# Kernel tuning notes

Measured on AMD Instinct MI355X. Metric: run time of the kernel, lower is better.

## Reference

```python
import jax, jax.numpy as jnp
import numpy as np

D_IN = 1024
D_OUT = 1024
H = 16


def setup_inputs() -> dict:
    key = jax.random.key(0)
    ks = jax.random.split(key, 11)
    B, Tq, Tk = 2, 2048, 2048
    s = 1.0 / np.sqrt(D_IN)
    return {
        "q": jax.random.normal(ks[0], (B, Tq, D_IN), jnp.float32),
        "k": jax.random.normal(ks[1], (B, Tk, D_IN), jnp.float32),
        "v": jax.random.normal(ks[2], (B, Tk, D_IN), jnp.float32),
        "Wq": jax.random.uniform(ks[3], (D_IN, D_OUT), jnp.float32, -s, s),
        "bq": jax.random.uniform(ks[4], (D_OUT,), jnp.float32, -s, s),
        "Wk": jax.random.uniform(ks[5], (D_IN, D_OUT), jnp.float32, -s, s),
        "bk": jax.random.uniform(ks[6], (D_OUT,), jnp.float32, -s, s),
        "Wv": jax.random.uniform(ks[7], (D_IN, D_OUT), jnp.float32, -s, s),
        "bv": jax.random.uniform(ks[8], (D_OUT,), jnp.float32, -s, s),
        "Wo": jax.random.uniform(ks[9], (D_OUT, D_OUT), jnp.float32, -s, s),
        "bo": jax.random.uniform(ks[10], (D_OUT,), jnp.float32, -s, s),
    }


def reference(q, k, v, Wq, bq, Wk, bk, Wv, bv, Wo, bo):
    B, Tq, _ = q.shape
    Tk = k.shape[1]
    hd = D_OUT // H
    # QKV projections, split heads -> [B, H, T, hd]
    qh = (q @ Wq + bq).reshape(B, Tq, H, hd).transpose(0, 2, 1, 3)
    kh = (k @ Wk + bk).reshape(B, Tk, H, hd).transpose(0, 2, 1, 3)
    vh = (v @ Wv + bv).reshape(B, Tk, H, hd).transpose(0, 2, 1, 3)
    # scaled dot-product attention (scale uses key dim = head_dim)
    scores = jnp.einsum("bhqd,bhkd->bhqk", qh, kh) / jnp.sqrt(jnp.float32(hd))
    attn = jax.nn.softmax(scores, axis=-1)
    x = jnp.einsum("bhqk,bhkd->bhqd", attn, vh)
    x = x.transpose(0, 2, 1, 3).reshape(B, Tq, D_OUT)
    return x @ Wo + bo
```

## Files before the change

### kernel.cpp

```cpp
#include <hip/hip_runtime.h>
#include <hip/hip_bf16.h>

typedef __attribute__((ext_vector_type(8))) short short8;
typedef __attribute__((ext_vector_type(4))) short short4v;
typedef __attribute__((ext_vector_type(4))) float f32x4;

__device__ __forceinline__ unsigned short f2bf(float f) {
    __hip_bfloat16 h = __float2bfloat16(f);
    unsigned short u;
    __builtin_memcpy(&u, &h, 2);
    return u;
}
__device__ __forceinline__ short4v pack4bf(float a, float b, float c, float d) {
    union { __hip_bfloat162 h[2]; short4v s; } r;
    r.h[0] = __float22bfloat162_rn(make_float2(a, b));
    r.h[1] = __float22bfloat162_rn(make_float2(c, d));
    return r.s;
}
union cat8 { short4v h[2]; short8 v8; };

#define GLD16(gp, lp) __builtin_amdgcn_global_load_lds( \
    (const __attribute__((address_space(1))) void*)(gp), \
    (__attribute__((address_space(3))) void*)(lp), 16, 0, 0)

#define PHASE(WAITN) do { \
        asm volatile("s_waitcnt vmcnt(" #WAITN ")" ::: "memory"); \
        __builtin_amdgcn_s_barrier(); \
        asm volatile("" ::: "memory"); \
        __builtin_amdgcn_sched_barrier(0); } while (0)

__global__ __launch_bounds__(256) void prep(
    const float* __restrict__ q, const float* __restrict__ k, const float* __restrict__ v,
    unsigned short* __restrict__ qb, unsigned short* __restrict__ kb, unsigned short* __restrict__ vb,
    const float* __restrict__ W0, const float* __restrict__ W1,
    const float* __restrict__ W2, const float* __restrict__ W3,
    unsigned short* __restrict__ T0, unsigned short* __restrict__ T1,
    unsigned short* __restrict__ T2, unsigned short* __restrict__ T3)
{
    __shared__ unsigned short Ts[64 * 68];
    int bx = blockIdx.x;
    if (bx < 6144) {
        const float* src; unsigned short* dst;
        switch (bx >> 11) { case 0: src = q; dst = qb; break;
                            case 1: src = k; dst = kb; break;
                            default: src = v; dst = vb; break; }
        size_t i = ((size_t)(bx & 2047) * 256 + threadIdx.x) * 8;
        float4 x0 = *(const float4*)&src[i];
        float4 x1 = *(const float4*)&src[i + 4];
        union { unsigned short s[8]; uint4 u; } p;
        p.s[0] = f2bf(x0.x); p.s[1] = f2bf(x0.y); p.s[2] = f2bf(x0.z); p.s[3] = f2bf(x0.w);
        p.s[4] = f2bf(x1.x); p.s[5] = f2bf(x1.y); p.s[6] = f2bf(x1.z); p.s[7] = f2bf(x1.w);
        *(uint4*)&dst[i] = p.u;
        return;
    }
    int w = bx - 6144;
    int z = w >> 8, rem = w & 255;
    int kx = rem >> 4, ny = rem & 15;
    const float* W;
    unsigned short* T;
    switch (z) {
        case 0: W = W0; T = T0; break;
        case 1: W = W1; T = T1; break;
        case 2: W = W2; T = T2; break;
        default: W = W3; T = T3; break;
    }
    int tid = threadIdx.x;
    int c = tid & 7, r = tid >> 3;
    int k0 = kx * 64, n0 = ny * 64;
    for (int i = 0; i < 64; i += 32) {
        const float* src = &W[(size_t)(k0 + r + i) * 1024 + n0 + c * 8];
        float4 x0 = *(const float4*)src;
        float4 x1 = *(const float4*)(src + 4);
        unsigned short* d = &Ts[(r + i) * 68 + c * 8];
        d[0] = f2bf(x0.x); d[1] = f2bf(x0.y); d[2] = f2bf(x0.z); d[3] = f2bf(x0.w);
        d[4] = f2bf(x1.x); d[5] = f2bf(x1.y); d[6] = f2bf(x1.z); d[7] = f2bf(x1.w);
    }
    __syncthreads();
    for (int i = 0; i < 64; i += 32) {
        union { unsigned short s[8]; uint4 v; } u;
        for (int j = 0; j < 8; j++) u.s[j] = Ts[(c * 8 + j) * 68 + (r + i)];
        *(uint4*)&T[(size_t)(n0 + r + i) * 1024 + k0 + c * 8] = u.v;
    }
}

__device__ __forceinline__ void gemm_core_p(
    const unsigned short* __restrict__ A, const unsigned short* __restrict__ BT,
    const float* __restrict__ bias, unsigned short* __restrict__ out16,
    int mode, float scale)
{
    const int K = 1024;
    __shared__ unsigned short As[3][128 * 32];
    __shared__ unsigned short Bs[3][128 * 32];
    int tid = threadIdx.x;
    int m0 = blockIdx.x * 128, n0 = blockIdx.y * 128;
    int lane = tid & 63, wave = tid >> 6;
    int lm = lane & 15, quad = lane >> 4;
    int wm = (wave >> 1) * 64, wn = (wave & 1) * 64;

    int lrow = lane >> 2;
    int scol = ((lane & 3) ^ ((lane >> 3) & 3)) * 8;
    const unsigned short* Ag = A + (size_t)(m0 + wave * 32 + lrow) * K + scol;
    const unsigned short* Bg = BT + (size_t)(n0 + wave * 32 + lrow) * K + scol;

    int rpos = (quad ^ ((lm >> 1) & 3)) * 8;

    f32x4 acc[4][4];
    for (int i = 0; i < 4; i++)
        for (int j = 0; j < 4; j++)
            for (int r = 0; r < 4; r++) acc[i][j][r] = 0.0f;

#define GSTAGE(BUF) do { \
        GLD16(Ag,          &As[BUF][(wave * 32) * 32]); \
        GLD16(Ag + 16 * K, &As[BUF][(wave * 32 + 16) * 32]); \
        GLD16(Bg,          &Bs[BUF][(wave * 32) * 32]); \
        GLD16(Bg + 16 * K, &Bs[BUF][(wave * 32 + 16) * 32]); \
        Ag += 32; Bg += 32; } while (0)

#define GCOMP(BUF) do { \
        short8 a[4], b[4]; \
        _Pragma("unroll") \
        for (int i = 0; i < 4; i++) \
            a[i] = *(const short8*)&As[BUF][(wm + i * 16 + lm) * 32 + rpos]; \
        _Pragma("unroll") \
        for (int j = 0; j < 4; j++) \
            b[j] = *(const short8*)&Bs[BUF][(wn + j * 16 + lm) * 32 + rpos]; \
        _Pragma("unroll") \
        for (int i = 0; i < 4; i++) \
            _Pragma("unroll") \
            for (int j = 0; j < 4; j++) \
                acc[i][j] = __builtin_amdgcn_mfma_f32_16x16x32_bf16(a[i], b[j], acc[i][j], 0, 0, 0); \
        } while (0)

    GSTAGE(0); GSTAGE(1);
    for (int u = 0; u < 10; u++) {
        PHASE(4); GSTAGE(2); GCOMP(0);
        PHASE(4); GSTAGE(0); GCOMP(1);
        PHASE(4); GSTAGE(1); GCOMP(2);
    }
    PHASE(4); GCOMP(0);
    PHASE(0); GCOMP(1);

#undef GSTAGE
#undef GCOMP

    for (int j = 0; j < 4; j++) {
        int col = n0 + wn + j * 16 + lm;
        float bv = bias[col];
        for (int i = 0; i < 4; i++) {
            int rowb = m0 + wm + i * 16 + quad * 4;
            int h = col >> 6, d = col & 63;
            int bb = rowb >> 11, t = rowb & 2047;
            if (mode == 1) {
                size_t base = (((size_t)(bb * 16 + h)) * 2048 + t) * 64 + d;
                for (int r = 0; r < 4; r++)
                    out16[base + (size_t)r * 64] = f2bf((acc[i][j][r] + bv) * scale);
            } else {
                ushort4 pk;
                pk.x = f2bf((acc[i][j][0] + bv) * scale);
                pk.y = f2bf((acc[i][j][1] + bv) * scale);
                pk.z = f2bf((acc[i][j][2] + bv) * scale);
                pk.w = f2bf((acc[i][j][3] + bv) * scale);
                *(ushort4*)&out16[(((size_t)(bb * 16 + h)) * 64 + d) * 2048 + t] = pk;
            }
        }
    }
}

__global__ __launch_bounds__(256, 3) void qkv_gemm(
    const unsigned short* __restrict__ qbf, const unsigned short* __restrict__ kbf,
    const unsigned short* __restrict__ vbf,
    const unsigned short* __restrict__ WqT, const unsigned short* __restrict__ WkT,
    const unsigned short* __restrict__ WvT,
    const float* __restrict__ bq, const float* __restrict__ bk, const float* __restrict__ bv,
    unsigned short* __restrict__ Qh, unsigned short* __restrict__ Kh,
    unsigned short* __restrict__ VhT)
{
    switch (blockIdx.z) {
        case 0:  gemm_core_p(qbf, WqT, bq, Qh,  1, 0.18033688011f); break;
        case 1:  gemm_core_p(kbf, WkT, bk, Kh,  1, 1.0f);           break;
        default: gemm_core_p(vbf, WvT, bv, VhT, 2, 1.0f);           break;
    }
}

__global__ __launch_bounds__(256, 2) void out_gemm(
    const unsigned short* __restrict__ A, const unsigned short* __restrict__ BT,
    const float* __restrict__ bias, float* __restrict__ out)
{
    const int K = 1024;
    __shared__ unsigned short As[3][128 * 32];
    __shared__ unsigned short Bs[3][64 * 32];
    int tid = threadIdx.x;
    int m0 = blockIdx.x * 128, n0 = blockIdx.y * 64;
    int lane = tid & 63, wave = tid >> 6;
    int lm = lane & 15, quad = lane >> 4;
    int wm = wave * 32;

    int lrow = lane >> 2;
    int scol = ((lane & 3) ^ ((lane >> 3) & 3)) * 8;
    const unsigned short* Ag = A + (size_t)(m0 + wave * 32 + lrow) * K + scol;
    const unsigned short* Bg = BT + (size_t)(n0 + wave * 16 + lrow) * K + scol;

    int rpos = (quad ^ ((lm >> 1) & 3)) * 8;

    f32x4 acc[2][4];
    for (int i = 0; i < 2; i++)
        for (int j = 0; j < 4; j++)
            for (int r = 0; r < 4; r++) acc[i][j][r] = 0.0f;

#define OSTAGE(BUF) do { \
        GLD16(Ag,          &As[BUF][(wave * 32) * 32]); \
        GLD16(Ag + 16 * K, &As[BUF][(wave * 32 + 16) * 32]); \
        GLD16(Bg,          &Bs[BUF][(wave * 16) * 32]); \
        Ag += 32; Bg += 32; } while (0)

#define OCOMP(BUF) do { \
        short8 a[2], b[4]; \
        _Pragma("unroll") \
        for (int i = 0; i < 2; i++) \
            a[i] = *(const short8*)&As[BUF][(wm + i * 16 + lm) * 32 + rpos]; \
        _Pragma("unroll") \
        for (int j = 0; j < 4; j++) \
            b[j] = *(const short8*)&Bs[BUF][(j * 16 + lm) * 32 + rpos]; \
        _Pragma("unroll") \
        for (int i = 0; i < 2; i++) \
            _Pragma("unroll") \
            for (int j = 0; j < 4; j++) \
                acc[i][j] = __builtin_amdgcn_mfma_f32_16x16x32_bf16(a[i], b[j], acc[i][j], 0, 0, 0); \
        } while (0)

    OSTAGE(0); OSTAGE(1);
    for (int u = 0; u < 10; u++) {
        PHASE(3); OSTAGE(2); OCOMP(0);
        PHASE(3); OSTAGE(0); OCOMP(1);
        PHASE(3); OSTAGE(1); OCOMP(2);
    }
    PHASE(3); OCOMP(0);
    PHASE(0); OCOMP(1);

#undef OSTAGE
#undef OCOMP

    for (int j = 0; j < 4; j++) {
        int col = n0 + j * 16 + lm;
        float bv = bias[col];
        for (int i = 0; i < 2; i++) {
            int rowb = m0 + wm + i * 16 + quad * 4;
            for (int r = 0; r < 4; r++)
                out[(size_t)(rowb + r) * 1024 + col] = acc[i][j][r] + bv;
        }
    }
}

__global__ __launch_bounds__(256) void attn_kernel(
    const unsigned short* __restrict__ Qh, const unsigned short* __restrict__ Kh,
    const unsigned short* __restrict__ VhT, unsigned short* __restrict__ X)
{
    __shared__ unsigned short Ks[4][64 * 64];
    __shared__ unsigned short Vt[4][64 * 64];

    int tid = threadIdx.x;
    int qblk = blockIdx.x & 15, bh = blockIdx.x >> 4;
    int b = bh >> 4, h = bh & 15;
    int lane = tid & 63, wave = tid >> 6;
    int lm = lane & 15, quad = lane >> 4;

    const unsigned short* Kbase = Kh + (size_t)bh * 2048 * 64;
    const unsigned short* Vbase = VhT + (size_t)bh * 64 * 2048;

    int srow = wave * 8 + (lane >> 3);
    int schk = ((lane & 7) ^ ((lane >> 3) & 7)) * 8;
    int swz  = lm & 7;

    const char* ks0 = (const char*)&Ks[0][0] + lm * 128 + ((quad ^ swz) * 16);
    const char* ks1 = (const char*)&Ks[0][0] + lm * 128 + (((quad + 4) ^ swz) * 16);
    int qh2 = quad >> 1, wo = (quad & 1) * 8;
    const char* vt0 = (const char*)&Vt[0][0] + lm * 128 + (((0 + qh2) ^ swz) * 16) + wo;
    const char* vt1 = (const char*)&Vt[0][0] + lm * 128 + (((2 + qh2) ^ swz) * 16) + wo;
    const char* vt2 = (const char*)&Vt[0][0] + lm * 128 + (((4 + qh2) ^ swz) * 16) + wo;
    const char* vt3 = (const char*)&Vt[0][0] + lm * 128 + (((6 + qh2) ^ swz) * 16) + wo;

    const unsigned short* Kg = Kbase + (size_t)srow * 64 + schk;
    const unsigned short* Vg = Vbase + (size_t)srow * 2048 + schk;

    int qrow = qblk * 128 + wave * 32 + lm;
    const unsigned short* qptr = Qh + ((size_t)bh * 2048 + qrow) * 64;
    short8 qfa0 = *(const short8*)&qptr[quad * 8];
    short8 qfa1 = *(const short8*)&qptr[32 + quad * 8];
    short8 qfb0 = *(const short8*)&qptr[16 * 64 + quad * 8];
    short8 qfb1 = *(const short8*)&qptr[16 * 64 + 32 + quad * 8];
    asm volatile("s_waitcnt vmcnt(0)" ::: "memory");

    f32x4 oA[4], oB[4];
    for (int n = 0; n < 4; n++)
        for (int r = 0; r < 4; r++) { oA[n][r] = 0.0f; oB[n][r] = 0.0f; }
    float lA = 0.0f, lB = 0.0f;
    f32x4 zf;
    zf[0] = zf[1] = zf[2] = zf[3] = 0.0f;

#define STAGE(BUF) do { \
        GLD16(Kg,             &Ks[BUF][(wave * 8) * 64]); \
        GLD16(Kg + 32 * 64,   &Ks[BUF][(32 + wave * 8) * 64]); \
        GLD16(Vg,             &Vt[BUF][(wave * 8) * 64]); \
        GLD16(Vg + 32 * 2048, &Vt[BUF][(32 + wave * 8) * 64]); \
        Kg += 64 * 64; Vg += 64; } while (0)

#define QKPV(CUR) do { \
        short4v pa[4], pb[4]; \
        _Pragma("unroll") \
        for (int t = 0; t < 4; t++) { \
            short8 ka0 = *(const short8*)(ks0 + (CUR) * 8192 + t * 2048); \
            short8 ka1 = *(const short8*)(ks1 + (CUR) * 8192 + t * 2048); \
            f32x4 za = __builtin_amdgcn_mfma_f32_16x16x32_bf16(ka0, qfa0, zf, 0, 0, 0); \
            za = __builtin_amdgcn_mfma_f32_16x16x32_bf16(ka1, qfa1, za, 0, 0, 0); \
            f32x4 zb = __builtin_amdgcn_mfma_f32_16x16x32_bf16(ka0, qfb0, zf, 0, 0, 0); \
            zb = __builtin_amdgcn_mfma_f32_16x16x32_bf16(ka1, qfb1, zb, 0, 0, 0); \
            float a0 = __builtin_amdgcn_exp2f(za[0]); \
            float a1 = __builtin_amdgcn_exp2f(za[1]); \
            float a2 = __builtin_amdgcn_exp2f(za[2]); \
            float a3 = __builtin_amdgcn_exp2f(za[3]); \
            lA += (a0 + a1) + (a2 + a3); \
            pa[t] = pack4bf(a0, a1, a2, a3); \
            float b0 = __builtin_amdgcn_exp2f(zb[0]); \
            float b1 = __builtin_amdgcn_exp2f(zb[1]); \
            float b2 = __builtin_amdgcn_exp2f(zb[2]); \
            float b3 = __builtin_amdgcn_exp2f(zb[3]); \
            lB += (b0 + b1) + (b2 + b3); \
            pb[t] = pack4bf(b0, b1, b2, b3); \
        } \
        cat8 pA0, pA1, pB0, pB1; \
        pA0.h[0] = pa[0]; pA0.h[1] = pa[1]; \
        pA1.h[0] = pa[2]; pA1.h[1] = pa[3]; \
        pB0.h[0] = pb[0]; pB0.h[1] = pb[1]; \
        pB1.h[0] = pb[2]; pB1.h[1] = pb[3]; \
        _Pragma("unroll") \
        for (int n = 0; n < 4; n++) { \
            cat8 v01, v23; \
            v01.h[0] = *(const short4v*)(vt0 + (CUR) * 8192 + n * 2048); \
            v01.h[1] = *(const short4v*)(vt1 + (CUR) * 8192 + n * 2048); \
            v23.h[0] = *(const short4v*)(vt2 + (CUR) * 8192 + n * 2048); \
            v23.h[1] = *(const short4v*)(vt3 + (CUR) * 8192 + n * 2048); \
            oA[n] = __builtin_amdgcn_mfma_f32_16x16x32_bf16(pA0.v8, v01.v8, oA[n], 0, 0, 0); \
            oB[n] = __builtin_amdgcn_mfma_f32_16x16x32_bf16(pB0.v8, v01.v8, oB[n], 0, 0, 0); \
            oA[n] = __builtin_amdgcn_mfma_f32_16x16x32_bf16(pA1.v8, v23.v8, oA[n], 0, 0, 0); \
            oB[n] = __builtin_amdgcn_mfma_f32_16x16x32_bf16(pB1.v8, v23.v8, oB[n], 0, 0, 0); \
        } } while (0)

    STAGE(0); STAGE(1); STAGE(2);

    for (int u = 0; u < 7; u++) {
        PHASE(8); STAGE(3); QKPV(0);
        PHASE(8); STAGE(0); QKPV(1);
        PHASE(8); STAGE(1); QKPV(2);
        PHASE(8); STAGE(2); QKPV(3);
    }
    PHASE(8); STAGE(3); QKPV(0);
    PHASE(8); QKPV(1);
    PHASE(4); QKPV(2);
    PHASE(0); QKPV(3);

#undef STAGE
#undef QKPV

    lA += __shfl_xor(lA, 16);
    lA += __shfl_xor(lA, 32);
    lB += __shfl_xor(lB, 16);
    lB += __shfl_xor(lB, 32);
    float invA = 1.0f / lA;
    float invB = 1.0f / lB;

    for (int r = 0; r < 4; r++) {
        int src = (lane & 48) | (quad * 4 + r);
        float invAr = __shfl(invA, src);
        float invBr = __shfl(invB, src);
        int rowA = qblk * 128 + wave * 32 + quad * 4 + r;
        for (int n = 0; n < 4; n++) {
            X[((size_t)b * 2048 + rowA) * 1024 + h * 64 + n * 16 + lm] = f2bf(oA[n][r] * invAr);
            X[((size_t)b * 2048 + rowA + 16) * 1024 + h * 64 + n * 16 + lm] = f2bf(oB[n][r] * invBr);
        }
    }
}

extern "C" void kernel_launch(void* const* d_in, const int* in_sizes, int n_in,
                              void* d_out, int out_size, void* d_ws, size_t ws_size,
                              hipStream_t stream)
{
    const float* q  = (const float*)d_in[0];
    const float* k  = (const float*)d_in[1];
    const float* v  = (const float*)d_in[2];
    const float* Wq = (const float*)d_in[3];
    const float* bq = (const float*)d_in[4];
    const float* Wk = (const float*)d_in[5];
    const float* bk = (const float*)d_in[6];
    const float* Wv = (const float*)d_in[7];
    const float* bv = (const float*)d_in[8];
    const float* Wo = (const float*)d_in[9];
    const float* bo = (const float*)d_in[10];

    unsigned short* ws  = (unsigned short*)d_ws;
    const unsigned int M1 = 1u << 20;
    unsigned short* WqT = ws;
    unsigned short* WkT = ws + M1;
    unsigned short* WvT = ws + 2 * M1;
    unsigned short* WoT = ws + 3 * M1;
    unsigned short* qbf = ws + 4 * M1;
    unsigned short* kbf = ws + 8 * M1;
    unsigned short* vbf = ws + 12 * M1;
    unsigned short* Qh  = ws + 16 * M1;
    unsigned short* Kh  = ws + 4 * M1;
    unsigned short* VhT = ws + 8 * M1;
    unsigned short* X   = ws + 12 * M1;

    prep<<<dim3(7168), 256, 0, stream>>>(q, k, v, qbf, kbf, vbf,
                                         Wq, Wk, Wv, Wo, WqT, WkT, WvT, WoT);
    qkv_gemm<<<dim3(32, 8, 3), 256, 0, stream>>>(qbf, kbf, vbf, WqT, WkT, WvT,
                                                 bq, bk, bv, Qh, Kh, VhT);
    attn_kernel<<<dim3(512), 256, 0, stream>>>(Qh, Kh, VhT, X);
    out_gemm<<<dim3(32, 16), 256, 0, stream>>>(X, WoT, bo, (float*)d_out);
}
```

Baseline: 218.4 us.

## Software-pipeline QK^T of next tile with PV of current tile

Splits the fused per-tile QK/softmax/PV step into separate QK and PV stages and staggers them, so the QK^T and exp of tile i+1 is issued alongside the PV MFMAs of tile i. K and V loads are split into separate stage macros, with V staged one tile behind K and wait counts adjusted. The aim is to hide exp and MFMA dependency latency by interleaving independent work. In exchange it keeps two sets of packed P registers live, which raises register pressure and could lower occupancy.

```diff
diff --git a/kernel.cpp b/kernel.cpp
--- a/kernel.cpp
+++ b/kernel.cpp
@@ -279,8 +279,8 @@
     const char* vt2 = (const char*)&Vt[0][0] + lm * 128 + (((4 + qh2) ^ swz) * 16) + wo;
     const char* vt3 = (const char*)&Vt[0][0] + lm * 128 + (((6 + qh2) ^ swz) * 16) + wo;
 
-    const unsigned short* Kg = Kbase + (size_t)srow * 64 + schk;
-    const unsigned short* Vg = Vbase + (size_t)srow * 2048 + schk;
+    const unsigned short* Kg0 = Kbase + (size_t)srow * 64 + schk;
+    const unsigned short* Vg0 = Vbase + (size_t)srow * 2048 + schk;
 
     int qrow = qblk * 128 + wave * 32 + lm;
     const unsigned short* qptr = Qh + ((size_t)bh * 2048 + qrow) * 64;
@@ -297,69 +297,77 @@
     f32x4 zf;
     zf[0] = zf[1] = zf[2] = zf[3] = 0.0f;
 
-#define STAGE(BUF) do { \
-        GLD16(Kg,             &Ks[BUF][(wave * 8) * 64]); \
-        GLD16(Kg + 32 * 64,   &Ks[BUF][(32 + wave * 8) * 64]); \
-        GLD16(Vg,             &Vt[BUF][(wave * 8) * 64]); \
-        GLD16(Vg + 32 * 2048, &Vt[BUF][(32 + wave * 8) * 64]); \
-        Kg += 64 * 64; Vg += 64; } while (0)
-
-#define QKPV(CUR) do { \
-        short4v pa[4], pb[4]; \
-        _Pragma("unroll") \
-        for (int t = 0; t < 4; t++) { \
-            short8 ka0 = *(const short8*)(ks0 + (CUR) * 8192 + t * 2048); \
-            short8 ka1 = *(const short8*)(ks1 + (CUR) * 8192 + t * 2048); \
-            f32x4 za = __builtin_amdgcn_mfma_f32_16x16x32_bf16(ka0, qfa0, zf, 0, 0, 0); \
-            za = __builtin_amdgcn_mfma_f32_16x16x32_bf16(ka1, qfa1, za, 0, 0, 0); \
-            f32x4 zb = __builtin_amdgcn_mfma_f32_16x16x32_bf16(ka0, qfb0, zf, 0, 0, 0); \
-            zb = __builtin_amdgcn_mfma_f32_16x16x32_bf16(ka1, qfb1, zb, 0, 0, 0); \
-            float a0 = __builtin_amdgcn_exp2f(za[0]); \
-            float a1 = __builtin_amdgcn_exp2f(za[1]); \
-            float a2 = __builtin_amdgcn_exp2f(za[2]); \
-            float a3 = __builtin_amdgcn_exp2f(za[3]); \
-            lA += (a0 + a1) + (a2 + a3); \
-            pa[t] = pack4bf(a0, a1, a2, a3); \
-            float b0 = __builtin_amdgcn_exp2f(zb[0]); \
-            float b1 = __builtin_amdgcn_exp2f(zb[1]); \
-            float b2 = __builtin_amdgcn_exp2f(zb[2]); \
-            float b3 = __builtin_amdgcn_exp2f(zb[3]); \
-            lB += (b0 + b1) + (b2 + b3); \
-            pb[t] = pack4bf(b0, b1, b2, b3); \
-        } \
-        cat8 pA0, pA1, pB0, pB1; \
-        pA0.h[0] = pa[0]; pA0.h[1] = pa[1]; \
-        pA1.h[0] = pa[2]; pA1.h[1] = pa[3]; \
-        pB0.h[0] = pb[0]; pB0.h[1] = pb[1]; \
-        pB1.h[0] = pb[2]; pB1.h[1] = pb[3]; \
+    cat8 xA0, xA1, xB0, xB1;
+    cat8 yA0, yA1, yB0, yB1;
+
+#define STK(T, BUF) do { \
+        GLD16(Kg0 + (size_t)(T) * 4096,        &Ks[BUF][(wave * 8) * 64]); \
+        GLD16(Kg0 + (size_t)(T) * 4096 + 2048, &Ks[BUF][(32 + wave * 8) * 64]); } while (0)
+
+#define STV(T, BUF) do { \
+        GLD16(Vg0 + (T) * 64,             &Vt[BUF][(wave * 8) * 64]); \
+        GLD16(Vg0 + (T) * 64 + 32 * 2048, &Vt[BUF][(32 + wave * 8) * 64]); } while (0)
+
+#define QKT(CUR, T, DSTA, DSTB) do { \
+        short8 ka0 = *(const short8*)(ks0 + (CUR) * 8192 + (T) * 2048); \
+        short8 ka1 = *(const short8*)(ks1 + (CUR) * 8192 + (T) * 2048); \
+        f32x4 za = __builtin_amdgcn_mfma_f32_16x16x32_bf16(ka0, qfa0, zf, 0, 0, 0); \
+        za = __builtin_amdgcn_mfma_f32_16x16x32_bf16(ka1, qfa1, za, 0, 0, 0); \
+        f32x4 zb = __builtin_amdgcn_mfma_f32_16x16x32_bf16(ka0, qfb0, zf, 0, 0, 0); \
+        zb = __builtin_amdgcn_mfma_f32_16x16x32_bf16(ka1, qfb1, zb, 0, 0, 0); \
+        float a0 = __builtin_amdgcn_exp2f(za[0]); \
+        float a1 = __builtin_amdgcn_exp2f(za[1]); \
+        float a2 = __builtin_amdgcn_exp2f(za[2]); \
+        float a3 = __builtin_amdgcn_exp2f(za[3]); \
+        lA += (a0 + a1) + (a2 + a3); \
+        DSTA = pack4bf(a0, a1, a2, a3); \
+        float b0 = __builtin_amdgcn_exp2f(zb[0]); \
+        float b1 = __builtin_amdgcn_exp2f(zb[1]); \
+        float b2 = __builtin_amdgcn_exp2f(zb[2]); \
+        float b3 = __builtin_amdgcn_exp2f(zb[3]); \
+        lB += (b0 + b1) + (b2 + b3); \
+        DSTB = pack4bf(b0, b1, b2, b3); } while (0)
+
+#define QK(CUR, S) do { \
+        QKT(CUR, 0, S##A0.h[0], S##B0.h[0]); \
+        QKT(CUR, 1, S##A0.h[1], S##B0.h[1]); \
+        QKT(CUR, 2, S##A1.h[0], S##B1.h[0]); \
+        QKT(CUR, 3, S##A1.h[1], S##B1.h[1]); } while (0)
+
+#define PV(VBUF, S) do { \
         _Pragma("unroll") \
         for (int n = 0; n < 4; n++) { \
             cat8 v01, v23; \
-            v01.h[0] = *(const short4v*)(vt0 + (CUR) * 8192 + n * 2048); \
-            v01.h[1] = *(const short4v*)(vt1 + (CUR) * 8192 + n * 2048); \
-            v23.h[0] = *(const short4v*)(vt2 + (CUR) * 8192 + n * 2048); \
-            v23.h[1] = *(const short4v*)(vt3 + (CUR) * 8192 + n * 2048); \
-            oA[n] = __builtin_amdgcn_mfma_f32_16x16x32_bf16(pA0.v8, v01.v8, oA[n], 0, 0, 0); \
-            oB[n] = __builtin_amdgcn_mfma_f32_16x16x32_bf16(pB0.v8, v01.v8, oB[n], 0, 0, 0); \
-            oA[n] = __builtin_amdgcn_mfma_f32_16x16x32_bf16(pA1.v8, v23.v8, oA[n], 0, 0, 0); \
-            oB[n] = __builtin_amdgcn_mfma_f32_16x16x32_bf16(pB1.v8, v23.v8, oB[n], 0, 0, 0); \
+            v01.h[0] = *(const short4v*)(vt0 + (VBUF) * 8192 + n * 2048); \
+            v01.h[1] = *(const short4v*)(vt1 + (VBUF) * 8192 + n * 2048); \
+            v23.h[0] = *(const short4v*)(vt2 + (VBUF) * 8192 + n * 2048); \
+            v23.h[1] = *(const short4v*)(vt3 + (VBUF) * 8192 + n * 2048); \
+            oA[n] = __builtin_amdgcn_mfma_f32_16x16x32_bf16(S##A0.v8, v01.v8, oA[n], 0, 0, 0); \
+            oB[n] = __builtin_amdgcn_mfma_f32_16x16x32_bf16(S##B0.v8, v01.v8, oB[n], 0, 0, 0); \
+            oA[n] = __builtin_amdgcn_mfma_f32_16x16x32_bf16(S##A1.v8, v23.v8, oA[n], 0, 0, 0); \
+            oB[n] = __builtin_amdgcn_mfma_f32_16x16x32_bf16(S##B1.v8, v23.v8, oB[n], 0, 0, 0); \
         } } while (0)
 
-    STAGE(0); STAGE(1); STAGE(2);
-
-    for (int u = 0; u < 7; u++) {
-        PHASE(8); STAGE(3); QKPV(0);
-        PHASE(8); STAGE(0); QKPV(1);
-        PHASE(8); STAGE(1); QKPV(2);
-        PHASE(8); STAGE(2); QKPV(3);
-    }
-    PHASE(8); STAGE(3); QKPV(0);
-    PHASE(8); QKPV(1);
-    PHASE(4); QKPV(2);
-    PHASE(0); QKPV(3);
-
-#undef STAGE
-#undef QKPV
+    STK(0, 0); STK(1, 1); STV(0, 0); STK(2, 2); STV(1, 1);
+
+    PHASE(8); STK(3, 3); STV(2, 2); QK(0, x);
+
+    for (int w = 0; w < 7; w++) {
+        PHASE(8); STK(4 * w + 4, 0); STV(4 * w + 3, 3); QK(1, y); PV(0, x);
+        PHASE(8); STK(4 * w + 5, 1); STV(4 * w + 4, 0); QK(2, x); PV(1, y);
+        PHASE(8); STK(4 * w + 6, 2); STV(4 * w + 5, 1); QK(3, y); PV(2, x);
+        PHASE(8); STK(4 * w + 7, 3); STV(4 * w + 6, 2); QK(0, x); PV(3, y);
+    }
+    PHASE(8); STV(31, 3); QK(1, y); PV(0, x);
+    PHASE(6); QK(2, x); PV(1, y);
+    PHASE(2); QK(3, y); PV(2, x);
+    PHASE(0); PV(3, y);
+
+#undef STK
+#undef STV
+#undef QKT
+#undef QK
+#undef PV
 
     lA += __shfl_xor(lA, 16);
     lA += __shfl_xor(lA, 32);
```

Measured after the change: 236.7 us. 8.4% more time.
